# Optimization experiments

Hardware: AMD Instinct MI355X
Metric: run time of the kernel (lower is better)

The kernel has to match this reference:

```python
import jax, jax.numpy as jnp
import numpy as np

INPUT_DIM = 1024
HIDDEN_DIM = 64  # per-head dim
NUM_HEADS = 16
LN_EPS = 1e-5


def setup_inputs() -> dict:
    key = jax.random.key(0)
    ks = jax.random.split(key, 12)
    B, S, D = 2, 2048, INPUT_DIM
    HD = HIDDEN_DIM * NUM_HEADS
    s_in = 1.0 / np.sqrt(D)
    s_hd = 1.0 / np.sqrt(HD)
    return {
        "x": jax.random.normal(ks[0], (B, S, D), dtype=jnp.float32),
        "Wq": jax.random.normal(ks[1], (D, HD), dtype=jnp.float32) * s_in,
        "bq": jax.random.normal(ks[2], (HD,), dtype=jnp.float32) * 0.02,
        "Wk": jax.random.normal(ks[3], (D, HD), dtype=jnp.float32) * s_in,
        "bk": jax.random.normal(ks[4], (HD,), dtype=jnp.float32) * 0.02,
        "Wv": jax.random.normal(ks[5], (D, HD), dtype=jnp.float32) * s_in,
        "bv": jax.random.normal(ks[6], (HD,), dtype=jnp.float32) * 0.02,
        "Wo": jax.random.normal(ks[7], (HD, D), dtype=jnp.float32) * s_hd,
        "bo": jax.random.normal(ks[8], (D,), dtype=jnp.float32) * 0.02,
        "gamma": jnp.ones((D,), dtype=jnp.float32),
        "beta": jnp.zeros((D,), dtype=jnp.float32),
    }


def _layer_norm(y, gamma, beta):
    mu = jnp.mean(y, axis=-1, keepdims=True)
    var = jnp.mean(jnp.square(y - mu), axis=-1, keepdims=True)
    return (y - mu) * jax.lax.rsqrt(var + LN_EPS) * gamma + beta


def reference(x, Wq, bq, Wk, bk, Wv, bv, Wo, bo, gamma, beta):
    B, S, D = x.shape
    H, Hd = NUM_HEADS, HIDDEN_DIM
    # Faithful to the torch module: (B,S,H*Hd) -> reshape (B,H,S,Hd) WITHOUT transpose.
    Q = (x @ Wq + bq).reshape(B, H, S, Hd)
    K = (x @ Wk + bk).reshape(B, H, S, Hd)
    V = (x @ Wv + bv).reshape(B, H, S, Hd)
    scores = jnp.einsum("bhqd,bhkd->bhqk", Q, K) / jnp.sqrt(jnp.float32(Hd))
    attn = jax.nn.softmax(scores, axis=-1)  # dropout=0 -> identity
    ctx = jnp.einsum("bhqk,bhkd->bhqd", attn, V).reshape(B, S, H * Hd)
    out = _layer_norm(x + (ctx @ Wo + bo), gamma, beta)
    return jax.nn.gelu(out, approximate=False)
```

## Files before the change

### kernel.cpp

```cpp
#include <hip/hip_runtime.h>
#include <hip/hip_bf16.h>
#include <cstdint>
#include <cstddef>


#define SEQ   2048
#define DIM   1024
#define NHEAD 16
#define HDIM  64
#define ROWS  4096

#define QSCALE 0.1803368801111204f

typedef __attribute__((ext_vector_type(8))) __bf16 bf16x8;
typedef __attribute__((ext_vector_type(4))) float floatx4;
typedef __attribute__((ext_vector_type(8))) unsigned short ushortx8;

__device__ __forceinline__ unsigned short f2bf(float f) {
  unsigned int u = __float_as_uint(f);
  u += 0x7FFFu + ((u >> 16) & 1u);
  return (unsigned short)(u >> 16);
}

__device__ __forceinline__ unsigned int pk2bf(float a, float b) {
  float2 f; f.x = a; f.y = b;
  __hip_bfloat162 h = __float22bfloat162_rn(f);
  return *(unsigned int*)&h;
}

__device__ __forceinline__ void glds16(const unsigned short* g,
                                       unsigned short* l) {
  __builtin_amdgcn_global_load_lds(
      (const __attribute__((address_space(1))) void*)g,
      (__attribute__((address_space(3))) void*)l, 16, 0, 0);
}

__global__ __launch_bounds__(256) void cvt_bf16(const float* __restrict__ in,
                                                unsigned short* __restrict__ out,
                                                int n4) {
  int i = blockIdx.x * 256 + threadIdx.x;
  if (i >= n4) return;
  float4 v = ((const float4*)in)[i];
  ushort4 o;
  o.x = f2bf(v.x); o.y = f2bf(v.y); o.z = f2bf(v.z); o.w = f2bf(v.w);
  ((ushort4*)out)[i] = o;
}

__global__ __launch_bounds__(256) void transpose_w4(
    const float* __restrict__ Wq, const float* __restrict__ Wk,
    const float* __restrict__ Wv, const float* __restrict__ Wo,
    unsigned short* __restrict__ Wqkvt, unsigned short* __restrict__ Wot) {
  __shared__ float t[32][33];
  const int z = blockIdx.z;
  const float* in = (z == 0) ? Wq : (z == 1) ? Wk : (z == 2) ? Wv : Wo;
  unsigned short* out = (z < 3) ? Wqkvt + (size_t)z * DIM * DIM : Wot;
  const int bx = blockIdx.x * 32, by = blockIdx.y * 32;
  const int tx = threadIdx.x, ty = threadIdx.y;
#pragma unroll
  for (int i = ty; i < 32; i += 8)
    t[i][tx] = in[(size_t)(by + i) * DIM + bx + tx];
  __syncthreads();
#pragma unroll
  for (int i = ty; i < 32; i += 8)
    out[(size_t)(bx + i) * DIM + by + tx] = f2bf(t[tx][i]);
}

__global__ __launch_bounds__(256) void transpose_v(
    const unsigned short* __restrict__ Vb,
    unsigned short* __restrict__ VbT) {
  __shared__ unsigned short t[64][65];
  const int bh = blockIdx.y;
  const int s0 = blockIdx.x * 64;
  const int tx = threadIdx.x;
  const int ty = threadIdx.y;
  const unsigned short* src = Vb + (size_t)bh * (SEQ * HDIM);
  unsigned short* dst = VbT + (size_t)bh * (SEQ * HDIM);
#pragma unroll
  for (int i = ty; i < 64; i += 4)
    t[i][tx] = src[(size_t)(s0 + i) * HDIM + tx];
  __syncthreads();
#pragma unroll
  for (int i = ty; i < 64; i += 4)
    dst[(size_t)i * SEQ + s0 + tx] = t[tx][i];
}

__global__ __launch_bounds__(256) void swizzle_kv(
    unsigned short* __restrict__ Kb,
    const unsigned short* __restrict__ VbT,
    unsigned short* __restrict__ Vs) {
  __shared__ unsigned short t[64 * 72];
  const int tile = blockIdx.x;
  const int bh   = blockIdx.y;
  const int isV  = blockIdx.z;
  const int tid  = threadIdx.x;
  const size_t slab = (size_t)bh * (SEQ * HDIM);
  if (!isV) {
    const unsigned short* src = Kb + slab + (size_t)tile * 4096;
#pragma unroll
    for (int p = 0; p < 2; ++p) {
      const int c = p * 256 + tid;
      const int row = c >> 3, col = (c & 7) * 8;
      *(ushortx8*)&t[row * 72 + col] = *(const ushortx8*)&src[c * 8];
    }
  } else {
    const unsigned short* src = VbT + slab;
#pragma unroll
    for (int p = 0; p < 2; ++p) {
      const int c = p * 256 + tid;
      const int row = c >> 3, col = (c & 7) * 8;
      *(ushortx8*)&t[row * 72 + col] =
          *(const ushortx8*)&src[(size_t)row * SEQ + tile * 64 + col];
    }
  }
  __syncthreads();
  unsigned short* dst = (isV ? Vs : Kb) + slab + (size_t)tile * 4096;
  const int lane = tid & 63, wave = tid >> 6;
  const int l16 = lane & 15, quad = lane >> 4;
#pragma unroll
  for (int f = wave * 2; f < wave * 2 + 2; ++f) {
    const int step = f >> 2, g = f & 3;
    *(ushortx8*)&dst[f * 512 + lane * 8] =
        *(const ushortx8*)&t[(g * 16 + l16) * 72 + step * 32 + quad * 8];
  }
}

__global__ __launch_bounds__(256, 3) void gemm_qkv(
    const unsigned short* __restrict__ A,
    const unsigned short* __restrict__ Wt,
    const float* __restrict__ bq, const float* __restrict__ bk,
    const float* __restrict__ bv,
    unsigned short* __restrict__ Qb, unsigned short* __restrict__ Kb,
    unsigned short* __restrict__ Vb) {
  constexpr int K = DIM;
  __shared__ unsigned short As[128 * 64];
  __shared__ unsigned short Bs[128 * 64];
  const int tid  = threadIdx.x;
  const int lane = tid & 63, wave = tid >> 6;
  const int l16  = lane & 15, quad = lane >> 4;
  const int wm   = (wave & 1) * 64, wn = (wave >> 1) * 64;
  const int tm   = blockIdx.y * 128, tn = blockIdx.x * 128;
  const int grow = lane >> 3, gcol = (lane & 7) * 8;

  floatx4 acc[4][4] = {};

  for (int k0 = 0; k0 < K; k0 += 64) {
    __syncthreads();
#pragma unroll
    for (int p = 0; p < 4; ++p) {
      const int q = wave * 4 + p;
      const int row = q * 8 + grow;
      glds16(&A [(size_t)(tm + row) * K + k0 + gcol], &As[q * 512]);
      glds16(&Wt[(size_t)(tn + row) * K + k0 + gcol], &Bs[q * 512]);
    }
    __syncthreads();
#pragma unroll
    for (int step = 0; step < 2; ++step) {
      const int kk = step * 32 + quad * 8;
      bf16x8 af[4], bfr[4];
#pragma unroll
      for (int i = 0; i < 4; ++i)
        af[i] = *(const bf16x8*)&As[(wm + i * 16 + l16) * 64 + kk];
#pragma unroll
      for (int j = 0; j < 4; ++j)
        bfr[j] = *(const bf16x8*)&Bs[(wn + j * 16 + l16) * 64 + kk];
#pragma unroll
      for (int i = 0; i < 4; ++i)
#pragma unroll
        for (int j = 0; j < 4; ++j)
          acc[i][j] = __builtin_amdgcn_mfma_f32_16x16x32_bf16(af[i], bfr[j],
                                                              acc[i][j], 0, 0, 0);
    }
  }

#pragma unroll
  for (int j = 0; j < 4; ++j) {
    const int ng  = tn + wn + j * 16 + l16;
    const int seg = ng >> 10;
    const int col = ng & 1023;
    const float* bp    = (seg == 0) ? bq : (seg == 1) ? bk : bv;
    unsigned short* op = (seg == 0) ? Qb : (seg == 1) ? Kb : Vb;
    const float bias = bp[col];
    const float scl  = (seg == 0) ? QSCALE : 1.0f;
#pragma unroll
    for (int i = 0; i < 4; ++i) {
      const int m0 = tm + wm + i * 16 + quad * 4;
#pragma unroll
      for (int r = 0; r < 4; ++r)
        op[(size_t)(m0 + r) * DIM + col] = f2bf((acc[i][j][r] + bias) * scl);
    }
  }
}

__global__ __launch_bounds__(256) void gemm_o(
    const unsigned short* __restrict__ A,
    const unsigned short* __restrict__ Wt,
    const float* __restrict__ bo,
    float* __restrict__ Y) {
  constexpr int K = DIM;
  __shared__ unsigned short As[128 * 64];
  __shared__ unsigned short Bs[64 * 64];
  const int tid  = threadIdx.x;
  const int lane = tid & 63, wave = tid >> 6;
  const int l16  = lane & 15, quad = lane >> 4;
  const int wm   = wave * 32;
  const int tm   = blockIdx.y * 128, tn = blockIdx.x * 64;
  const int grow = lane >> 3, gcol = (lane & 7) * 8;

  floatx4 acc[2][4] = {};

  for (int k0 = 0; k0 < K; k0 += 64) {
    __syncthreads();
#pragma unroll
    for (int p = 0; p < 4; ++p) {
      const int q = wave * 4 + p;
      const int row = q * 8 + grow;
      glds16(&A[(size_t)(tm + row) * K + k0 + gcol], &As[q * 512]);
    }
#pragma unroll
    for (int p = 0; p < 2; ++p) {
      const int q = wave * 2 + p;
      const int row = q * 8 + grow;
      glds16(&Wt[(size_t)(tn + row) * K + k0 + gcol], &Bs[q * 512]);
    }
    __syncthreads();
#pragma unroll
    for (int step = 0; step < 2; ++step) {
      const int kk = step * 32 + quad * 8;
      bf16x8 af[2], bfr[4];
#pragma unroll
      for (int i = 0; i < 2; ++i)
        af[i] = *(const bf16x8*)&As[(wm + i * 16 + l16) * 64 + kk];
#pragma unroll
      for (int j = 0; j < 4; ++j)
        bfr[j] = *(const bf16x8*)&Bs[(j * 16 + l16) * 64 + kk];
#pragma unroll
      for (int i = 0; i < 2; ++i)
#pragma unroll
        for (int j = 0; j < 4; ++j)
          acc[i][j] = __builtin_amdgcn_mfma_f32_16x16x32_bf16(af[i], bfr[j],
                                                              acc[i][j], 0, 0, 0);
    }
  }

#pragma unroll
  for (int j = 0; j < 4; ++j) {
    const int n = tn + j * 16 + l16;
    const float bias = bo[n];
#pragma unroll
    for (int i = 0; i < 2; ++i) {
      const int m0 = tm + wm + i * 16 + quad * 4;
#pragma unroll
      for (int r = 0; r < 4; ++r)
        Y[(size_t)(m0 + r) * DIM + n] = acc[i][j][r] + bias;
    }
  }
}

__global__ __launch_bounds__(128) void attn_fwd(
    const unsigned short* __restrict__ Qb,
    const unsigned short* __restrict__ Ks,
    const unsigned short* __restrict__ Vs,
    unsigned short* __restrict__ ctx) {
  __shared__ unsigned short Pl[2][32 * 72];

  const int tid  = threadIdx.x;
  const int lane = tid & 63, wave = tid >> 6;
  const int l16  = lane & 15, quad = lane >> 4;
  const size_t slab = (size_t)blockIdx.y * SEQ * HDIM;
  const unsigned short* Q  = Qb + slab;
  const unsigned short* Kf = Ks + slab;
  const unsigned short* Vf = Vs + slab;
  const int q0 = blockIdx.x * 64 + wave * 32;

  bf16x8 qf[2][2];
#pragma unroll
  for (int h = 0; h < 2; ++h) {
    qf[h][0] = *(const bf16x8*)&Q[(size_t)(q0 + h * 16 + l16) * HDIM + quad * 8];
    qf[h][1] = *(const bf16x8*)&Q[(size_t)(q0 + h * 16 + l16) * HDIM + 32 + quad * 8];
  }

  floatx4 o[2][4] = {};
  float lr[2] = {0.f, 0.f};

  for (int tile = 0; tile < SEQ / 64; ++tile) {
    const unsigned short* kb = Kf + (size_t)tile * 4096;
    const unsigned short* vb = Vf + (size_t)tile * 4096;
    bf16x8 kf[2][4], vf[2][4];
#pragma unroll
    for (int step = 0; step < 2; ++step)
#pragma unroll
      for (int g = 0; g < 4; ++g) {
        kf[step][g] = *(const bf16x8*)&kb[(step * 4 + g) * 512 + lane * 8];
        vf[step][g] = *(const bf16x8*)&vb[(step * 4 + g) * 512 + lane * 8];
      }

    floatx4 s[2][4] = {};
#pragma unroll
    for (int step = 0; step < 2; ++step)
#pragma unroll
      for (int mt = 0; mt < 4; ++mt) {
        s[0][mt] = __builtin_amdgcn_mfma_f32_16x16x32_bf16(kf[step][mt], qf[0][step], s[0][mt], 0, 0, 0);
        s[1][mt] = __builtin_amdgcn_mfma_f32_16x16x32_bf16(kf[step][mt], qf[1][step], s[1][mt], 0, 0, 0);
      }

#pragma unroll
    for (int h = 0; h < 2; ++h) {
#pragma unroll
      for (int mt = 0; mt < 4; ++mt) {
        float p0 = __builtin_amdgcn_exp2f(s[h][mt][0]);
        float p1 = __builtin_amdgcn_exp2f(s[h][mt][1]);
        float p2 = __builtin_amdgcn_exp2f(s[h][mt][2]);
        float p3 = __builtin_amdgcn_exp2f(s[h][mt][3]);
        lr[h] += (p0 + p1) + (p2 + p3);
        uint2 pv;
        pv.x = pk2bf(p0, p1);
        pv.y = pk2bf(p2, p3);
        *(uint2*)&Pl[wave][(h * 16 + l16) * 72 + mt * 16 + quad * 4] = pv;
      }
    }
    __asm__ __volatile__("s_waitcnt lgkmcnt(0)" ::: "memory");

#pragma unroll
    for (int step = 0; step < 2; ++step) {
      const int kk = step * 32 + quad * 8;
      bf16x8 pf0 = *(const bf16x8*)&Pl[wave][(l16) * 72 + kk];
      bf16x8 pf1 = *(const bf16x8*)&Pl[wave][(16 + l16) * 72 + kk];
#pragma unroll
      for (int j = 0; j < 4; ++j) {
        o[0][j] = __builtin_amdgcn_mfma_f32_16x16x32_bf16(pf0, vf[step][j], o[0][j], 0, 0, 0);
        o[1][j] = __builtin_amdgcn_mfma_f32_16x16x32_bf16(pf1, vf[step][j], o[1][j], 0, 0, 0);
      }
    }
  }

#pragma unroll
  for (int h = 0; h < 2; ++h) {
    lr[h] += __shfl_xor(lr[h], 16, 64);
    lr[h] += __shfl_xor(lr[h], 32, 64);
  }
  unsigned short* cp = ctx + slab;
#pragma unroll
  for (int h = 0; h < 2; ++h) {
    float lb[4];
#pragma unroll
    for (int r = 0; r < 4; ++r)
      lb[r] = 1.0f / __shfl(lr[h], quad * 4 + r, 64);
#pragma unroll
    for (int j = 0; j < 4; ++j)
#pragma unroll
      for (int r = 0; r < 4; ++r)
        cp[(size_t)(q0 + h * 16 + quad * 4 + r) * HDIM + j * 16 + l16] =
            f2bf(o[h][j][r] * lb[r]);
  }
}

__global__ __launch_bounds__(256) void ln_gelu(
    const float* __restrict__ x, const float* __restrict__ y,
    const float* __restrict__ gamma, const float* __restrict__ beta,
    float* __restrict__ out) {
  const int row = blockIdx.x;
  const int tid = threadIdx.x;
  const float4 xv = ((const float4*)(x + (size_t)row * DIM))[tid];
  const float4 yv = ((const float4*)(y + (size_t)row * DIM))[tid];
  float4 s;
  s.x = xv.x + yv.x; s.y = xv.y + yv.y; s.z = xv.z + yv.z; s.w = xv.w + yv.w;
  float sum = (s.x + s.y) + (s.z + s.w);
  float sq  = (s.x * s.x + s.y * s.y) + (s.z * s.z + s.w * s.w);
#pragma unroll
  for (int off = 1; off < 64; off <<= 1) {
    sum += __shfl_xor(sum, off, 64);
    sq  += __shfl_xor(sq, off, 64);
  }
  __shared__ float red[8];
  const int wave = tid >> 6, lane = tid & 63;
  if (lane == 0) { red[wave] = sum; red[wave + 4] = sq; }
  __syncthreads();
  sum = red[0] + red[1] + red[2] + red[3];
  sq  = red[4] + red[5] + red[6] + red[7];
  const float mu   = sum * (1.0f / DIM);
  const float var  = sq * (1.0f / DIM) - mu * mu;
  const float rstd = rsqrtf(var + 1e-5f);
  const float4 gv = ((const float4*)gamma)[tid];
  const float4 bv = ((const float4*)beta)[tid];
  float4 ov;
  {
    const float v = (s.x - mu) * rstd * gv.x + bv.x;
    ov.x = 0.5f * v * (1.0f + erff(v * 0.70710678118654752f));
  }
  {
    const float v = (s.y - mu) * rstd * gv.y + bv.y;
    ov.y = 0.5f * v * (1.0f + erff(v * 0.70710678118654752f));
  }
  {
    const float v = (s.z - mu) * rstd * gv.z + bv.z;
    ov.z = 0.5f * v * (1.0f + erff(v * 0.70710678118654752f));
  }
  {
    const float v = (s.w - mu) * rstd * gv.w + bv.w;
    ov.w = 0.5f * v * (1.0f + erff(v * 0.70710678118654752f));
  }
  ((float4*)(out + (size_t)row * DIM))[tid] = ov;
}

extern "C" void kernel_launch(void* const* d_in, const int* in_sizes, int n_in,
                              void* d_out, int out_size, void* d_ws, size_t ws_size,
                              hipStream_t stream) {
  (void)in_sizes; (void)n_in; (void)out_size; (void)ws_size;
  const float* x     = (const float*)d_in[0];
  const float* Wq    = (const float*)d_in[1];
  const float* bq    = (const float*)d_in[2];
  const float* Wk    = (const float*)d_in[3];
  const float* bk    = (const float*)d_in[4];
  const float* Wv    = (const float*)d_in[5];
  const float* bv    = (const float*)d_in[6];
  const float* Wo    = (const float*)d_in[7];
  const float* bo    = (const float*)d_in[8];
  const float* gamma = (const float*)d_in[9];
  const float* beta  = (const float*)d_in[10];
  float* out = (float*)d_out;

  char* ws = (char*)d_ws;
  const size_t MB = 1u << 20;
  unsigned short* xb    = (unsigned short*)(ws);
  unsigned short* Wqkvt = (unsigned short*)(ws + 8 * MB);
  unsigned short* Wot   = (unsigned short*)(ws + 14 * MB);
  unsigned short* Qb    = (unsigned short*)(ws + 16 * MB);
  unsigned short* Kb    = (unsigned short*)(ws + 24 * MB);
  unsigned short* VbT   = (unsigned short*)(ws + 32 * MB);
  unsigned short* Cx    = (unsigned short*)(ws + 32 * MB);
  unsigned short* Vb    = (unsigned short*)(ws + 40 * MB);
  unsigned short* Vs    = (unsigned short*)(ws + 40 * MB);
  float*          Y     = (float*)(ws + 48 * MB);

  cvt_bf16<<<(ROWS * DIM / 4 + 255) / 256, 256, 0, stream>>>(x, xb, ROWS * DIM / 4);
  transpose_w4<<<dim3(32, 32, 4), dim3(32, 8), 0, stream>>>(Wq, Wk, Wv, Wo, Wqkvt, Wot);

  gemm_qkv<<<dim3(24, 32), 256, 0, stream>>>(xb, Wqkvt, bq, bk, bv, Qb, Kb, Vb);
  transpose_v<<<dim3(SEQ / 64, 32), dim3(64, 4), 0, stream>>>(Vb, VbT);
  swizzle_kv<<<dim3(SEQ / 64, 32, 2), 256, 0, stream>>>(Kb, VbT, Vs);
  attn_fwd<<<dim3(32, 32), 128, 0, stream>>>(Qb, Kb, Vs, Cx);
  gemm_o<<<dim3(16, 32), 256, 0, stream>>>(Cx, Wot, bo, Y);
  ln_gelu<<<ROWS, 256, 0, stream>>>(x, Y, gamma, beta, out);
}
```

Baseline: 227.2 us.

## Split attention over KV halves with merge kernel and fuse V transpose into swizzle

```diff
diff --git a/kernel.cpp b/kernel.cpp
--- a/kernel.cpp
+++ b/kernel.cpp
@@ -65,62 +65,45 @@
     out[(size_t)(bx + i) * DIM + by + tx] = f2bf(t[tx][i]);
 }
 
-__global__ __launch_bounds__(256) void transpose_v(
-    const unsigned short* __restrict__ Vb,
-    unsigned short* __restrict__ VbT) {
-  __shared__ unsigned short t[64][65];
-  const int bh = blockIdx.y;
-  const int s0 = blockIdx.x * 64;
-  const int tx = threadIdx.x;
-  const int ty = threadIdx.y;
-  const unsigned short* src = Vb + (size_t)bh * (SEQ * HDIM);
-  unsigned short* dst = VbT + (size_t)bh * (SEQ * HDIM);
-#pragma unroll
-  for (int i = ty; i < 64; i += 4)
-    t[i][tx] = src[(size_t)(s0 + i) * HDIM + tx];
-  __syncthreads();
-#pragma unroll
-  for (int i = ty; i < 64; i += 4)
-    dst[(size_t)i * SEQ + s0 + tx] = t[tx][i];
-}
-
 __global__ __launch_bounds__(256) void swizzle_kv(
     unsigned short* __restrict__ Kb,
-    const unsigned short* __restrict__ VbT,
+    const unsigned short* __restrict__ Vb,
     unsigned short* __restrict__ Vs) {
   __shared__ unsigned short t[64 * 72];
   const int tile = blockIdx.x;
   const int bh   = blockIdx.y;
   const int isV  = blockIdx.z;
   const int tid  = threadIdx.x;
-  const size_t slab = (size_t)bh * (SEQ * HDIM);
-  if (!isV) {
-    const unsigned short* src = Kb + slab + (size_t)tile * 4096;
-#pragma unroll
-    for (int p = 0; p < 2; ++p) {
-      const int c = p * 256 + tid;
-      const int row = c >> 3, col = (c & 7) * 8;
-      *(ushortx8*)&t[row * 72 + col] = *(const ushortx8*)&src[c * 8];
-    }
-  } else {
-    const unsigned short* src = VbT + slab;
-#pragma unroll
-    for (int p = 0; p < 2; ++p) {
-      const int c = p * 256 + tid;
-      const int row = c >> 3, col = (c & 7) * 8;
-      *(ushortx8*)&t[row * 72 + col] =
-          *(const ushortx8*)&src[(size_t)row * SEQ + tile * 64 + col];
-    }
+  const size_t base = (size_t)bh * (SEQ * HDIM) + (size_t)tile * 4096;
+  const unsigned short* src = (isV ? Vb : Kb) + base;
+#pragma unroll
+  for (int p = 0; p < 2; ++p) {
+    const int c = p * 256 + tid;
+    *(ushortx8*)&t[(c >> 3) * 72 + (c & 7) * 8] = *(const ushortx8*)&src[c * 8];
   }
   __syncthreads();
-  unsigned short* dst = (isV ? Vs : Kb) + slab + (size_t)tile * 4096;
+  unsigned short* dst = (isV ? Vs : Kb) + base;
   const int lane = tid & 63, wave = tid >> 6;
   const int l16 = lane & 15, quad = lane >> 4;
-#pragma unroll
-  for (int f = wave * 2; f < wave * 2 + 2; ++f) {
-    const int step = f >> 2, g = f & 3;
-    *(ushortx8*)&dst[f * 512 + lane * 8] =
-        *(const ushortx8*)&t[(g * 16 + l16) * 72 + step * 32 + quad * 8];
+  if (!isV) {
+#pragma unroll
+    for (int p = 0; p < 2; ++p) {
+      const int f = wave * 2 + p;
+      const int step = f >> 2, g = f & 3;
+      *(ushortx8*)&dst[f * 512 + lane * 8] =
+          *(const ushortx8*)&t[(g * 16 + l16) * 72 + step * 32 + quad * 8];
+    }
+  } else {
+#pragma unroll
+    for (int p = 0; p < 2; ++p) {
+      const int f = wave * 2 + p;
+      const int step = f >> 2, g = f & 3;
+      ushortx8 v;
+#pragma unroll
+      for (int e = 0; e < 8; ++e)
+        v[e] = t[(step * 32 + quad * 8 + e) * 72 + g * 16 + l16];
+      *(ushortx8*)&dst[f * 512 + lane * 8] = v;
+    }
   }
 }
 
@@ -260,17 +243,23 @@
     const unsigned short* __restrict__ Qb,
     const unsigned short* __restrict__ Ks,
     const unsigned short* __restrict__ Vs,
-    unsigned short* __restrict__ ctx) {
+    unsigned short* __restrict__ Op0, unsigned short* __restrict__ Op1,
+    float* __restrict__ l0, float* __restrict__ l1) {
   __shared__ unsigned short Pl[2][32 * 72];
 
   const int tid  = threadIdx.x;
   const int lane = tid & 63, wave = tid >> 6;
   const int l16  = lane & 15, quad = lane >> 4;
-  const size_t slab = (size_t)blockIdx.y * SEQ * HDIM;
+  const int id   = blockIdx.x;
+  const int w    = id >> 3;
+  const int head = (id & 7) * 4 + (w & 3);
+  const int qt   = (w >> 2) & 31;
+  const int half = w >> 7;
+  const size_t slab = (size_t)head * SEQ * HDIM;
   const unsigned short* Q  = Qb + slab;
   const unsigned short* Kf = Ks + slab;
   const unsigned short* Vf = Vs + slab;
-  const int q0 = blockIdx.x * 64 + wave * 32;
+  const int q0 = qt * 64 + wave * 32;
 
   bf16x8 qf[2][2];
 #pragma unroll
@@ -282,7 +271,8 @@
   floatx4 o[2][4] = {};
   float lr[2] = {0.f, 0.f};
 
-  for (int tile = 0; tile < SEQ / 64; ++tile) {
+  for (int t = 0; t < 16; ++t) {
+    const int tile = half * 16 + t;
     const unsigned short* kb = Kf + (size_t)tile * 4096;
     const unsigned short* vb = Vf + (size_t)tile * 4096;
     bf16x8 kf[2][4], vf[2][4];
@@ -338,20 +328,38 @@
     lr[h] += __shfl_xor(lr[h], 16, 64);
     lr[h] += __shfl_xor(lr[h], 32, 64);
   }
-  unsigned short* cp = ctx + slab;
+  unsigned short* Op = half ? Op1 : Op0;
+  float*          lp = half ? l1 : l0;
 #pragma unroll
   for (int h = 0; h < 2; ++h) {
-    float lb[4];
-#pragma unroll
-    for (int r = 0; r < 4; ++r)
-      lb[r] = 1.0f / __shfl(lr[h], quad * 4 + r, 64);
+    if (quad == 0)
+      lp[head * SEQ + q0 + h * 16 + l16] = lr[h];
 #pragma unroll
     for (int j = 0; j < 4; ++j)
 #pragma unroll
       for (int r = 0; r < 4; ++r)
-        cp[(size_t)(q0 + h * 16 + quad * 4 + r) * HDIM + j * 16 + l16] =
-            f2bf(o[h][j][r] * lb[r]);
-  }
+        Op[slab + (size_t)(q0 + h * 16 + quad * 4 + r) * HDIM + j * 16 + l16] =
+            f2bf(o[h][j][r]);
+  }
+}
+
+__global__ __launch_bounds__(256) void attn_merge(
+    const unsigned short* __restrict__ Op0,
+    const unsigned short* __restrict__ Op1,
+    const float* __restrict__ l0, const float* __restrict__ l1,
+    unsigned short* __restrict__ Cx) {
+  const int i = blockIdx.x * 256 + threadIdx.x;
+  const float inv = 1.0f / (l0[i >> 3] + l1[i >> 3]);
+  ushortx8 a = *(const ushortx8*)&Op0[(size_t)i * 8];
+  ushortx8 b = *(const ushortx8*)&Op1[(size_t)i * 8];
+  ushortx8 o;
+#pragma unroll
+  for (int e = 0; e < 8; ++e) {
+    const float fa = __uint_as_float((unsigned int)a[e] << 16);
+    const float fb = __uint_as_float((unsigned int)b[e] << 16);
+    o[e] = f2bf((fa + fb) * inv);
+  }
+  *(ushortx8*)&Cx[(size_t)i * 8] = o;
 }
 
 __global__ __launch_bounds__(256) void ln_gelu(
@@ -422,23 +430,26 @@
   char* ws = (char*)d_ws;
   const size_t MB = 1u << 20;
   unsigned short* xb    = (unsigned short*)(ws);
+  unsigned short* Op0   = (unsigned short*)(ws);
   unsigned short* Wqkvt = (unsigned short*)(ws + 8 * MB);
+  float*          lp0   = (float*)(ws + 8 * MB);
+  float*          lp1   = (float*)(ws + 8 * MB + 256 * 1024);
   unsigned short* Wot   = (unsigned short*)(ws + 14 * MB);
   unsigned short* Qb    = (unsigned short*)(ws + 16 * MB);
   unsigned short* Kb    = (unsigned short*)(ws + 24 * MB);
-  unsigned short* VbT   = (unsigned short*)(ws + 32 * MB);
-  unsigned short* Cx    = (unsigned short*)(ws + 32 * MB);
+  unsigned short* Vs    = (unsigned short*)(ws + 32 * MB);
   unsigned short* Vb    = (unsigned short*)(ws + 40 * MB);
-  unsigned short* Vs    = (unsigned short*)(ws + 40 * MB);
+  unsigned short* Cx    = (unsigned short*)(ws + 40 * MB);
   float*          Y     = (float*)(ws + 48 * MB);
+  unsigned short* Op1   = (unsigned short*)(ws + 48 * MB);
 
   cvt_bf16<<<(ROWS * DIM / 4 + 255) / 256, 256, 0, stream>>>(x, xb, ROWS * DIM / 4);
   transpose_w4<<<dim3(32, 32, 4), dim3(32, 8), 0, stream>>>(Wq, Wk, Wv, Wo, Wqkvt, Wot);
 
   gemm_qkv<<<dim3(24, 32), 256, 0, stream>>>(xb, Wqkvt, bq, bk, bv, Qb, Kb, Vb);
-  transpose_v<<<dim3(SEQ / 64, 32), dim3(64, 4), 0, stream>>>(Vb, VbT);
-  swizzle_kv<<<dim3(SEQ / 64, 32, 2), 256, 0, stream>>>(Kb, VbT, Vs);
-  attn_fwd<<<dim3(32, 32), 128, 0, stream>>>(Qb, Kb, Vs, Cx);
+  swizzle_kv<<<dim3(SEQ / 64, 32, 2), 256, 0, stream>>>(Kb, Vb, Vs);
+  attn_fwd<<<2048, 128, 0, stream>>>(Qb, Kb, Vs, Op0, Op1, lp0, lp1);
+  attn_merge<<<(ROWS * DIM) / (8 * 256), 256, 0, stream>>>(Op0, Op1, lp0, lp1, Cx);
   gemm_o<<<dim3(16, 32), 256, 0, stream>>>(Cx, Wot, bo, Y);
   ln_gelu<<<ROWS, 256, 0, stream>>>(x, Y, gamma, beta, out);
 }
```

Result: faster. 220.4 us (-3.0%).
